# Optimization experiments

Hardware: AMD Instinct MI355X
Metric: run time of the kernel (lower is better)

The kernel has to match this reference:

```python
import jax, jax.numpy as jnp
import numpy as np

PI = jnp.pi

def phasor_encode(x):
    # map phase in [-1,1] to unit complex phasor exp(i*pi*x)
    return jnp.exp(jnp.complex64(1j) * PI * x.astype(jnp.float32))

def phasor_act(z):
    # angle of complex activation, normalized back to [-1,1]
    return jnp.angle(z) / PI

def multi_dense(x, w, b):
    # PhasorMultiDense: x [b,t,d], w [h,d,D], b [h,D] (complex bias, ones init)
    xz = phasor_encode(x)                                      # [b,t,d] complex64
    wz = w.astype(jnp.complex64)
    bz = b.astype(jnp.complex64)
    yz = jnp.einsum('btd,hdD->bhtD', xz, wz) + bz[None, :, None, :]
    return phasor_act(yz)                                      # [b,h,t,D] real

def attend(q, k, v):
    # VSA phasor attention: similarity = Re(qz . conj(kz)) / d, softmax, complex bundle of v phasors
    d = q.shape[-1]
    qz = phasor_encode(q)
    kz = phasor_encode(k)
    scores = jnp.real(jnp.einsum('bhtd,bhTd->bhtT', qz, jnp.conj(kz))) / d
    probs = jax.nn.softmax(scores, axis=-1)
    vz = phasor_encode(v)
    out = jnp.einsum('bhtT,bhTd->bhtd', probs.astype(jnp.complex64), vz)
    return phasor_act(out)                                     # [b,h,t,D]

def setup_inputs() -> dict:
    key = jax.random.key(0)
    ks = jax.random.split(key, 8)
    B, Tq, Tkv, D, H = 2, 1024, 1024, 512, 8
    sw = 1.0 / np.sqrt(D)       # VarianceScaling(1.0) fan_in
    swo = 1.0 / np.sqrt(H * D)
    return {
        'query': jax.random.uniform(ks[0], (B, Tq, D), jnp.float32, -1.0, 1.0),
        'keyvalue': jax.random.uniform(ks[1], (B, Tkv, D), jnp.float32, -1.0, 1.0),
        'wq': jax.random.normal(ks[2], (H, D, D), jnp.float32) * sw,
        'bq': jnp.ones((H, D), jnp.float32),
        'wk': jax.random.normal(ks[3], (H, D, D), jnp.float32) * sw,
        'bk': jnp.ones((H, D), jnp.float32),
        'wv': jax.random.normal(ks[4], (H, D, D), jnp.float32) * sw,
        'bv': jnp.ones((H, D), jnp.float32),
        'wo': jax.random.normal(ks[5], (H * D, D), jnp.float32) * swo,
        'bo': jnp.ones((D,), jnp.float32),
    }

def reference(query, keyvalue, wq, bq, wk, bk, wv, bv, wo, bo):
    q = multi_dense(query, wq, bq)        # [b,h,t,D]
    k = multi_dense(keyvalue, wk, bk)
    v = multi_dense(keyvalue, wv, bv)
    r = attend(q, k, v)                   # [b,h,t,D]
    b_, h_, t_, d_ = r.shape
    r_flat = jnp.transpose(r, (0, 2, 1, 3)).reshape(b_, t_, h_ * d_)  # b t (h d)
    # final PhasorDense
    xz = phasor_encode(r_flat)
    z = jnp.einsum('btd,dD->btD', xz, wo.astype(jnp.complex64)) + bo.astype(jnp.complex64)
    return phasor_act(z)                  # [b, t_q, output_channels]
```

## Files before the change

kernel.cpp:

```cpp
#include <hip/hip_runtime.h>
#include <math.h>


#define PI_F 3.14159274101257324f

typedef __attribute__((ext_vector_type(8))) _Float16 half8;
typedef __attribute__((ext_vector_type(4))) _Float16 half4;
typedef __attribute__((ext_vector_type(2))) _Float16 half2v;
typedef __attribute__((ext_vector_type(16))) float f32x16;
typedef unsigned int u32;

#define MFMA32(a, b, c) __builtin_amdgcn_mfma_f32_32x32x16_f16((a), (b), (c), 0, 0, 0)
#define ROWOF(r, ln) (((r) & 3) + 8 * ((r) >> 2) + 4 * ((ln) >> 5))

__device__ __forceinline__ void gll16(const void* g, void* l) {
    __builtin_amdgcn_global_load_lds(
        (const __attribute__((address_space(1))) u32*)g,
        (__attribute__((address_space(3))) u32*)l, 16, 0, 0);
}

__device__ __forceinline__ void split2(float x, _Float16& h, _Float16& l) {
    _Float16 hh = (_Float16)x;
    h = hh;
    l = (_Float16)((x - (float)hh) * 4096.0f);
}

__device__ __forceinline__ int xcdswz(int bid, int nwg) {
    const int cpx = nwg >> 3;
    return (bid & 7) * cpx + (bid >> 3);
}

__global__ __launch_bounds__(256) void encode_phasor(
    const float* __restrict__ xq, const float* __restrict__ xkv,
    _Float16* __restrict__ qch, _Float16* __restrict__ qcl,
    _Float16* __restrict__ qsh, _Float16* __restrict__ qsl,
    _Float16* __restrict__ kch, _Float16* __restrict__ kcl,
    _Float16* __restrict__ ksh, _Float16* __restrict__ ksl)
{
    const int mt = blockIdx.x, yh = blockIdx.y, zi = blockIdx.z;
    const float* x = zi ? xkv : xq;
    __shared__ char fb[32768];
    const int tid = threadIdx.x;
    const int row = tid >> 3, lc = tid & 7;
    const float* xr = x + (size_t)(mt * 32 + row) * 512 + yh * 256;
    for (int c = 0; c < 2; ++c) {
        if (c) __syncthreads();
        half8 hs[4][2];
#pragma unroll
        for (int g = 0; g < 2; ++g)
#pragma unroll
            for (int q = 0; q < 2; ++q) {
                float4 v = *(const float4*)(xr + c * 128 + lc * 16 + g * 8 + q * 4);
                float cc[4], ss[4];
                sincosf(PI_F * v.x, &ss[0], &cc[0]);
                sincosf(PI_F * v.y, &ss[1], &cc[1]);
                sincosf(PI_F * v.z, &ss[2], &cc[2]);
                sincosf(PI_F * v.w, &ss[3], &cc[3]);
#pragma unroll
                for (int e = 0; e < 4; ++e) {
                    _Float16 a, b;
                    split2(cc[e], a, b); hs[0][g][q * 4 + e] = a; hs[1][g][q * 4 + e] = b;
                    split2(ss[e], a, b); hs[2][g][q * 4 + e] = a; hs[3][g][q * 4 + e] = b;
                }
            }
#pragma unroll
        for (int p = 0; p < 4; ++p) {
            char* base = fb + p * 8192 + lc * 1024 + row * 16;
            *(half8*)(base) = hs[p][0];
            *(half8*)(base + 512) = hs[p][1];
        }
        __syncthreads();
#pragma unroll
        for (int w = 0; w < 8; ++w) {
            const int u = w * 256 + tid;
            const int p = u >> 9, rest = u & 511;
            const int f = rest >> 6, within = rest & 63;
            _Float16* op;
            if (zi) op = (p == 0) ? kch : (p == 1) ? kcl : (p == 2) ? ksh : ksl;
            else    op = (p == 0) ? qch : (p == 1) ? qcl : (p == 2) ? qsh : qsl;
            const size_t fragG = (size_t)mt * 32 + yh * 16 + c * 8 + f;
            *(half8*)(op + fragG * 512 + within * 8) =
                *(const half8*)(fb + p * 8192 + f * 1024 + within * 16);
        }
    }
}

__global__ __launch_bounds__(256) void tsplit64(
    const float* __restrict__ w, _Float16* __restrict__ th, _Float16* __restrict__ tl,
    int K, int N)
{
    const int kt = blockIdx.x, ntile = blockIdx.y, h = blockIdx.z;
    const int k0 = kt * 64, n0 = ntile * 64;
    __shared__ float T[64][65];
    const int tid = threadIdx.x;
    const float* wb = w + (size_t)h * K * N;
    {
        const int r = tid >> 4, c4 = (tid & 15) * 4;
#pragma unroll
        for (int rr = 0; rr < 64; rr += 16) {
            float4 v = *(const float4*)&wb[(size_t)(k0 + rr + r) * N + n0 + c4];
            T[rr + r][c4 + 0] = v.x; T[rr + r][c4 + 1] = v.y;
            T[rr + r][c4 + 2] = v.z; T[rr + r][c4 + 3] = v.w;
        }
    }
    __syncthreads();
    {
        const int n = n0 + (tid >> 2), kq = k0 + (tid & 3) * 16;
        half8 hv[2], lv[2];
#pragma unroll
        for (int q = 0; q < 16; ++q) {
            float f = T[kq - k0 + q][n - n0];
            _Float16 hh, ll; split2(f, hh, ll);
            hv[q >> 3][q & 7] = hh; lv[q >> 3][q & 7] = ll;
        }
        const size_t hb = (size_t)h * 512 * K;
        const size_t offA = hb + ((size_t)((n >> 5) * (K >> 4) + (kq >> 4))) * 512
                            + (n & 31) * 8;
        *(half8*)(th + offA) = hv[0]; *(half8*)(th + offA + 256) = hv[1];
        *(half8*)(tl + offA) = lv[0]; *(half8*)(tl + offA + 256) = lv[1];
    }
}

__global__ __launch_bounds__(256) void tsplit_qkv(
    const float* __restrict__ wq, const float* __restrict__ wk,
    const float* __restrict__ wv,
    _Float16* __restrict__ qh, _Float16* __restrict__ ql,
    _Float16* __restrict__ kh, _Float16* __restrict__ kl,
    _Float16* __restrict__ vh, _Float16* __restrict__ vl, int hcnt)
{
    const int tsel = blockIdx.z / hcnt, h = blockIdx.z % hcnt;
    const int kt = blockIdx.x, ntile = blockIdx.y;
    const int k0 = kt * 64, n0 = ntile * 64;
    const float* w = (tsel == 0) ? wq : (tsel == 1) ? wk : wv;
    _Float16* th = (tsel == 0) ? qh : (tsel == 1) ? kh : vh;
    _Float16* tl = (tsel == 0) ? ql : (tsel == 1) ? kl : vl;
    __shared__ float T[64][65];
    const int tid = threadIdx.x;
    const float* wb = w + (size_t)h * 262144;
    {
        const int r = tid >> 4, c4 = (tid & 15) * 4;
#pragma unroll
        for (int rr = 0; rr < 64; rr += 16) {
            float4 v = *(const float4*)&wb[(size_t)(k0 + rr + r) * 512 + n0 + c4];
            T[rr + r][c4 + 0] = v.x; T[rr + r][c4 + 1] = v.y;
            T[rr + r][c4 + 2] = v.z; T[rr + r][c4 + 3] = v.w;
        }
    }
    __syncthreads();
    {
        const int n = n0 + (tid >> 2), kq = k0 + (tid & 3) * 16;
        half8 hv[2], lv[2];
#pragma unroll
        for (int q = 0; q < 16; ++q) {
            float f = T[kq - k0 + q][n - n0];
            _Float16 hh, ll; split2(f, hh, ll);
            hv[q >> 3][q & 7] = hh; lv[q >> 3][q & 7] = ll;
        }
        const size_t hb = (size_t)h * 262144;
        const size_t offA = hb + ((size_t)((n >> 5) * 32 + (kq >> 4))) * 512 + (n & 31) * 8;
        *(half8*)(th + offA) = hv[0]; *(half8*)(th + offA + 256) = hv[1];
        *(half8*)(tl + offA) = lv[0]; *(half8*)(tl + offA + 256) = lv[1];
    }
}

__global__ __launch_bounds__(256, 2) void proj_qk(
    const _Float16* __restrict__ qch, const _Float16* __restrict__ qcl,
    const _Float16* __restrict__ qsh, const _Float16* __restrict__ qsl,
    const _Float16* __restrict__ kch, const _Float16* __restrict__ kcl,
    const _Float16* __restrict__ ksh, const _Float16* __restrict__ ksl,
    const _Float16* __restrict__ wqh, const _Float16* __restrict__ wql,
    const _Float16* __restrict__ wkh, const _Float16* __restrict__ wkl,
    const float* __restrict__ bq, const float* __restrict__ bk,
    _Float16* __restrict__ qzh, _Float16* __restrict__ qzl,
    _Float16* __restrict__ kzh, _Float16* __restrict__ kzl,
    int h0, int hcnt)
{
    const int inp = blockIdx.z;
    const _Float16* xch = inp ? kch : qch;
    const _Float16* xcl = inp ? kcl : qcl;
    const _Float16* xsh = inp ? ksh : qsh;
    const _Float16* xsl = inp ? ksl : qsl;
    const _Float16* wth = inp ? wkh : wqh;
    const _Float16* wtl = inp ? wkl : wql;
    const float* bias = inp ? bk : bq;
    _Float16* ozh = inp ? kzh : qzh;
    _Float16* ozl = inp ? kzl : qzl;

    const int m0 = blockIdx.x * 64;
    const int hc = blockIdx.y >> 2;
    const int n0 = (blockIdx.y & 3) * 128;
    __shared__ char lds[32768];
    const int tid = threadIdx.x, wv = tid >> 6, ln = tid & 63;
    const int wr = wv >> 1, wc = wv & 1, lm32 = ln & 31;

    const size_t abase = ((size_t)((m0 >> 5) + wr)) * 32 * 512 + ln * 8;
    const _Float16* pxc[2] = { xch + abase, xcl + abase };
    const _Float16* pxs[2] = { xsh + abase, xsl + abase };

    const char* spB[4]; int dpB[4];
#pragma unroll
    for (int u = 0; u < 4; ++u) {
        const int g = wv * 4 + u;
        const int jt = g >> 2, hl = (g >> 1) & 1, ks = g & 1;
        const _Float16* base = (hl ? wtl : wth) + (size_t)hc * 262144;
        spB[u] = (const char*)(base
                 + ((size_t)(((n0 + jt * 32) >> 5) * 32 + ks)) * 512 + ln * 8);
        dpB[u] = g * 1024;
    }

    f32x16 ach[2] = {}, acl[2] = {}, ash[2] = {}, asl[2] = {};

    auto LOADA = [&](int s, half8 (&ac)[2][2], half8 (&as)[2][2]) {
#pragma unroll
        for (int hl = 0; hl < 2; ++hl)
#pragma unroll
            for (int ks = 0; ks < 2; ++ks) {
                ac[hl][ks] = *(const half8*)(pxc[hl] + (2 * s + ks) * 512);
                as[hl][ks] = *(const half8*)(pxs[hl] + (2 * s + ks) * 512);
            }
    };
    auto STAGEB = [&](int s, int buf) {
#pragma unroll
        for (int u = 0; u < 4; ++u)
            gll16(spB[u] + (size_t)s * 2048, lds + buf + dpB[u]);
    };
    auto MSTEP = [&](int buf, half8 (&ac)[2][2], half8 (&as)[2][2]) {
        half8 w0[2][2], w1[2][2];
#pragma unroll
        for (int ks = 0; ks < 2; ++ks)
#pragma unroll
            for (int j = 0; j < 2; ++j) {
                const int gb = (wc * 2 + j) * 4 + ks;
                w0[ks][j] = *(const half8*)(lds + buf + gb * 1024 + ln * 16);
                w1[ks][j] = *(const half8*)(lds + buf + (gb + 2) * 1024 + ln * 16);
            }
        __builtin_amdgcn_s_setprio(1);
#pragma unroll
        for (int ks = 0; ks < 2; ++ks)
#pragma unroll
            for (int j = 0; j < 2; ++j) {
                ach[j] = MFMA32(ac[0][ks], w0[ks][j], ach[j]);
                acl[j] = MFMA32(ac[0][ks], w1[ks][j], acl[j]);
                acl[j] = MFMA32(ac[1][ks], w0[ks][j], acl[j]);
                ash[j] = MFMA32(as[0][ks], w0[ks][j], ash[j]);
                asl[j] = MFMA32(as[0][ks], w1[ks][j], asl[j]);
                asl[j] = MFMA32(as[1][ks], w0[ks][j], asl[j]);
            }
        __builtin_amdgcn_s_setprio(0);
    };

    half8 Ac0[2][2], As0[2][2], Ac1[2][2], As1[2][2];
    LOADA(0, Ac0, As0); STAGEB(0, 0);
    const int NS = 16;
    for (int s = 0; s < NS; s += 2) {
        __syncthreads();
        STAGEB(s + 1, 16384); LOADA(s + 1, Ac1, As1);
        MSTEP(0, Ac0, As0);
        __syncthreads();
        if (s + 2 < NS) { STAGEB(s + 2, 0); LOADA(s + 2, Ac0, As0); }
        MSTEP(16384, Ac1, As1);
    }

    const float LS = 1.0f / 4096.0f;
    const int b = m0 >> 10, tbase = m0 & 1023;
    const size_t zz = (size_t)(b * hcnt + hc);
    const size_t zb = zz << 20;
    __syncthreads();
#pragma unroll
    for (int p = 0; p < 2; ++p) {
        if (p) __syncthreads();
#pragma unroll
        for (int j = 0; j < 2; ++j) {
            const int nloc = wc * 64 + j * 32 + lm32;
            const float bval = bias[(size_t)(h0 + hc) * 512 + n0 + nloc];
            const int kk = 2 * nloc;
#pragma unroll
            for (int r = 0; r < 16; ++r) {
                const int mloc = wr * 32 + ROWOF(r, ln);
                float yc = ach[j][r] + acl[j][r] * LS + bval;
                float ys = ash[j][r] + asl[j][r] * LS;
                float inv = 1.0f / sqrtf(fmaxf(yc * yc + ys * ys, 1e-36f));
                _Float16 c_h, c_l, s_h, s_l;
                split2(yc * inv, c_h, c_l);
                split2(ys * inv, s_h, s_l);
                half2v pr;
                pr[0] = p ? c_l : c_h;
                pr[1] = p ? s_l : s_h;
                *(half2v*)(lds + ((mloc >> 5) * 16 + (kk >> 4)) * 1024
                    + (mloc & 31) * 16 + 512 * ((kk >> 3) & 1) + (kk & 7) * 2) = pr;
            }
        }
        __syncthreads();
        _Float16* op = p ? ozl : ozh;
#pragma unroll
        for (int w = 0; w < 8; ++w) {
            const int u = w * 256 + tid;
            const int f = u >> 6, within = u & 63;
            const int ms = f >> 4, kf = f & 15;
            *(half8*)(op + zb + (((size_t)(tbase >> 5) + ms) * 64 + (n0 >> 3) + kf) * 512
                      + within * 8) = *(const half8*)(lds + f * 1024 + within * 16);
        }
    }
}

__global__ __launch_bounds__(256, 2) void proj_v(
    const _Float16* __restrict__ xch, const _Float16* __restrict__ xcl,
    const _Float16* __restrict__ xsh, const _Float16* __restrict__ xsl,
    const _Float16* __restrict__ wth, const _Float16* __restrict__ wtl,
    const float* __restrict__ bias,
    _Float16* __restrict__ vc_h, _Float16* __restrict__ vc_l,
    _Float16* __restrict__ vs_h, _Float16* __restrict__ vs_l,
    int h0, int hcnt)
{
    const int m0 = blockIdx.x * 64;
    const int hc = blockIdx.y >> 2;
    const int n0 = (blockIdx.y & 3) * 128;
    __shared__ char lds[32768];
    const int tid = threadIdx.x, wv = tid >> 6, ln = tid & 63;
    const int wr = wv >> 1, wc = wv & 1, lm32 = ln & 31;

    const size_t abase = ((size_t)((m0 >> 5) + wr)) * 32 * 512 + ln * 8;
    const _Float16* pxc[2] = { xch + abase, xcl + abase };
    const _Float16* pxs[2] = { xsh + abase, xsl + abase };

    const char* spB[4]; int dpB[4];
#pragma unroll
    for (int u = 0; u < 4; ++u) {
        const int g = wv * 4 + u;
        const int jt = g >> 2, hl = (g >> 1) & 1, ks = g & 1;
        const _Float16* base = (hl ? wtl : wth) + (size_t)hc * 262144;
        spB[u] = (const char*)(base
                 + ((size_t)(((n0 + jt * 32) >> 5) * 32 + ks)) * 512 + ln * 8);
        dpB[u] = g * 1024;
    }

    f32x16 ach[2] = {}, acl[2] = {}, ash[2] = {}, asl[2] = {};

    auto LOADA = [&](int s, half8 (&ac)[2][2], half8 (&as)[2][2]) {
#pragma unroll
        for (int hl = 0; hl < 2; ++hl)
#pragma unroll
            for (int ks = 0; ks < 2; ++ks) {
                ac[hl][ks] = *(const half8*)(pxc[hl] + (2 * s + ks) * 512);
                as[hl][ks] = *(const half8*)(pxs[hl] + (2 * s + ks) * 512);
            }
    };
    auto STAGEB = [&](int s, int buf) {
#pragma unroll
        for (int u = 0; u < 4; ++u)
            gll16(spB[u] + (size_t)s * 2048, lds + buf + dpB[u]);
    };
    auto MSTEP = [&](int buf, half8 (&ac)[2][2], half8 (&as)[2][2]) {
        half8 w0[2][2], w1[2][2];
#pragma unroll
        for (int ks = 0; ks < 2; ++ks)
#pragma unroll
            for (int j = 0; j < 2; ++j) {
                const int gb = (wc * 2 + j) * 4 + ks;
                w0[ks][j] = *(const half8*)(lds + buf + gb * 1024 + ln * 16);
                w1[ks][j] = *(const half8*)(lds + buf + (gb + 2) * 1024 + ln * 16);
            }
        __builtin_amdgcn_s_setprio(1);
#pragma unroll
        for (int ks = 0; ks < 2; ++ks)
#pragma unroll
            for (int j = 0; j < 2; ++j) {
                ach[j] = MFMA32(ac[0][ks], w0[ks][j], ach[j]);
                acl[j] = MFMA32(ac[0][ks], w1[ks][j], acl[j]);
                acl[j] = MFMA32(ac[1][ks], w0[ks][j], acl[j]);
                ash[j] = MFMA32(as[0][ks], w0[ks][j], ash[j]);
                asl[j] = MFMA32(as[0][ks], w1[ks][j], asl[j]);
                asl[j] = MFMA32(as[1][ks], w0[ks][j], asl[j]);
            }
        __builtin_amdgcn_s_setprio(0);
    };

    half8 Ac0[2][2], As0[2][2], Ac1[2][2], As1[2][2];
    LOADA(0, Ac0, As0); STAGEB(0, 0);
    const int NS = 16;
    for (int s = 0; s < NS; s += 2) {
        __syncthreads();
        STAGEB(s + 1, 16384); LOADA(s + 1, Ac1, As1);
        MSTEP(0, Ac0, As0);
        __syncthreads();
        if (s + 2 < NS) { STAGEB(s + 2, 0); LOADA(s + 2, Ac0, As0); }
        MSTEP(16384, Ac1, As1);
    }

    const float LS = 1.0f / 4096.0f;
    const int b = m0 >> 10, tbase = m0 & 1023;
    const size_t zz = (size_t)(b * hcnt + hc);
    const size_t zvb = zz * 524288;
    _Float16* T = (_Float16*)lds;
#pragma unroll
    for (int p = 0; p < 4; ++p) {
        __syncthreads();
#pragma unroll
        for (int j = 0; j < 2; ++j) {
            const int dloc = wc * 64 + j * 32 + lm32;
            const float bval = bias[(size_t)(h0 + hc) * 512 + n0 + dloc];
#pragma unroll
            for (int r = 0; r < 16; ++r) {
                const int tloc = wr * 32 + ROWOF(r, ln);
                float yc = ach[j][r] + acl[j][r] * LS + bval;
                float ys = ash[j][r] + asl[j][r] * LS;
                float inv = 1.0f / sqrtf(fmaxf(yc * yc + ys * ys, 1e-36f));
                _Float16 hh, ll;
                if (p < 2) split2(yc * inv, hh, ll);
                else       split2(ys * inv, hh, ll);
                T[dloc * 80 + tloc] = (p & 1) ? ll : hh;
            }
        }
        __syncthreads();
        _Float16* op = (p == 0) ? vc_h : (p == 1) ? vc_l : (p == 2) ? vs_h : vs_l;
#pragma unroll
        for (int w = 0; w < 4; ++w) {
            const int u = w * 256 + tid;
            const int f = u >> 6, within = u & 63;
            const int ds_ = f >> 2, tf = f & 3;
            const int d = ds_ * 32 + (within & 31);
            const int tl = tf * 16 + (within >> 5) * 8;
            half8 vv = *(const half8*)(T + d * 80 + tl);
            *(half8*)(op + zvb + (((size_t)((n0 >> 5) + ds_)) * 64 + (tbase >> 4) + tf) * 512
                      + within * 8) = vv;
        }
    }
}

__global__ __launch_bounds__(256, 2) void scores_mfma(
    const _Float16* __restrict__ qzh, const _Float16* __restrict__ qzl,
    const _Float16* __restrict__ kzh, const _Float16* __restrict__ kzl,
    float* __restrict__ S, int Z)
{
    const int wg = xcdswz(blockIdx.x, Z * 64);
    const int z = wg >> 6;
    const int rem = wg & 63;
    const int m0 = (rem & 7) << 7, n0 = (rem >> 3) << 7;
    __shared__ char lds[32768];
    const size_t zb = (size_t)z << 20;
    const int tid = threadIdx.x, wv = tid >> 6, ln = tid & 63;
    const int wr = wv >> 1, wc = wv & 1, lm32 = ln & 31;

    const _Float16* pa[2] = { qzh + zb + ln * 8, qzl + zb + ln * 8 };
    const char* spB[4]; int dpB[4];
#pragma unroll
    for (int u = 0; u < 4; ++u) {
        const int g = wv * 4 + u;
        const int jt = g >> 2, hl = (g >> 1) & 1, ks = g & 1;
        spB[u] = (const char*)((hl ? kzl : kzh) + zb
                 + ((size_t)(((n0 + jt * 32) >> 5) * 64 + ks)) * 512 + ln * 8);
        dpB[u] = g * 1024;
    }

    f32x16 acch[2][2] = {}, accl[2][2] = {};

    auto LOADA = [&](int s, half8 (&a)[2][2][2]) {
#pragma unroll
        for (int hl = 0; hl < 2; ++hl)
#pragma unroll
            for (int i = 0; i < 2; ++i)
#pragma unroll
                for (int ks = 0; ks < 2; ++ks)
                    a[hl][i][ks] = *(const half8*)(pa[hl]
                        + ((size_t)((m0 >> 5) + wr * 2 + i) * 64 + 2 * s + ks) * 512);
    };
    auto STAGEB = [&](int s, int buf) {
#pragma unroll
        for (int u = 0; u < 4; ++u)
            gll16(spB[u] + (size_t)s * 2048, lds + buf + dpB[u]);
    };
    auto MSTEP = [&](int buf, half8 (&a)[2][2][2]) {
        half8 bh[2][2], bl[2][2];
#pragma unroll
        for (int ks = 0; ks < 2; ++ks)
#pragma unroll
            for (int j = 0; j < 2; ++j) {
                const int gb = (wc * 2 + j) * 4 + ks;
                bh[ks][j] = *(const half8*)(lds + buf + gb * 1024 + ln * 16);
                bl[ks][j] = *(const half8*)(lds + buf + (gb + 2) * 1024 + ln * 16);
            }
        __builtin_amdgcn_s_setprio(1);
#pragma unroll
        for (int ks = 0; ks < 2; ++ks)
#pragma unroll
            for (int i = 0; i < 2; ++i)
#pragma unroll
                for (int j = 0; j < 2; ++j) {
                    acch[i][j] = MFMA32(a[0][i][ks], bh[ks][j], acch[i][j]);
                    accl[i][j] = MFMA32(a[0][i][ks], bl[ks][j], accl[i][j]);
                    accl[i][j] = MFMA32(a[1][i][ks], bh[ks][j], accl[i][j]);
                }
        __builtin_amdgcn_s_setprio(0);
    };

    half8 A0[2][2][2], A1[2][2][2];
    LOADA(0, A0); STAGEB(0, 0);
    const int NS = 32;
    for (int s = 0; s < NS; s += 2) {
        __syncthreads();
        STAGEB(s + 1, 16384); LOADA(s + 1, A1);
        MSTEP(0, A0);
        __syncthreads();
        if (s + 2 < NS) { STAGEB(s + 2, 0); LOADA(s + 2, A0); }
        MSTEP(16384, A1);
    }
    const float LS = 1.0f / 4096.0f, SC = 1.0f / 512.0f;
#pragma unroll
    for (int i = 0; i < 2; ++i)
#pragma unroll
        for (int j = 0; j < 2; ++j)
#pragma unroll
            for (int r = 0; r < 16; ++r) {
                const int row = m0 + wr * 64 + i * 32 + ROWOF(r, ln);
                const int col = n0 + wc * 64 + j * 32 + lm32;
                S[zb + (size_t)row * 1024 + col] =
                    (acch[i][j][r] + accl[i][j][r] * LS) * SC;
            }
}

__global__ __launch_bounds__(256) void softmax_frag(
    const float* __restrict__ S, _Float16* __restrict__ Ph, _Float16* __restrict__ Pl)
{
    const int z = blockIdx.x >> 5, tt = blockIdx.x & 31;
    const float* Sb = S + ((size_t)z << 20) + ((size_t)tt << 15);
    const int tid = threadIdx.x;
    const int row = tid >> 3, lc = tid & 7;
    __shared__ float rsum[32];
    __shared__ char fb[32768];
    const float* prow = Sb + (size_t)row * 1024 + lc * 128;
    float s = 0.f;
    for (int q = 0; q < 32; ++q) {
        float4 v = *(const float4*)(prow + q * 4);
        s += (expf(v.x) + expf(v.y)) + (expf(v.z) + expf(v.w));
    }
    s += __shfl_xor(s, 1); s += __shfl_xor(s, 2); s += __shfl_xor(s, 4);
    if (lc == 0) rsum[row] = s;
    __syncthreads();
    const float inv = 1.0f / rsum[row];
    for (int c = 0; c < 4; ++c) {
        if (c) __syncthreads();
        const float* pc = Sb + (size_t)row * 1024 + c * 256 + lc * 32;
#pragma unroll
        for (int q = 0; q < 8; ++q) {
            float4 v = *(const float4*)(pc + q * 4);
            half4 hv, lv; _Float16 a, b;
            split2(expf(v.x) * inv, a, b); hv[0] = a; lv[0] = b;
            split2(expf(v.y) * inv, a, b); hv[1] = a; lv[1] = b;
            split2(expf(v.z) * inv, a, b); hv[2] = a; lv[2] = b;
            split2(expf(v.w) * inv, a, b); hv[3] = a; lv[3] = b;
            const int f = lc * 2 + (q >> 2);
            const int boff = f * 1024 + row * 16 + 512 * ((q >> 1) & 1) + (q & 1) * 8;
            *(half4*)(fb + boff) = hv;
            *(half4*)(fb + 16384 + boff) = lv;
        }
        __syncthreads();
#pragma unroll
        for (int w = 0; w < 8; ++w) {
            const int u = w * 256 + tid;
            const int pl = u >> 10, rest = u & 1023;
            const int f = rest >> 6, within = rest & 63;
            _Float16* dst = (pl ? Pl : Ph) + ((size_t)z << 20)
                          + ((size_t)(tt * 64 + c * 16 + f)) * 512 + within * 8;
            *(half8*)dst = *(const half8*)(fb + pl * 16384 + f * 1024 + within * 16);
        }
    }
}

__global__ __launch_bounds__(256, 2) void pv_mfma(
    const _Float16* __restrict__ Ph, const _Float16* __restrict__ Pl,
    const _Float16* __restrict__ vch, const _Float16* __restrict__ vcl,
    const _Float16* __restrict__ vsh, const _Float16* __restrict__ vsl,
    _Float16* __restrict__ rch, _Float16* __restrict__ rcl,
    _Float16* __restrict__ rsh, _Float16* __restrict__ rsl,
    int h0, int hcnt, int Z)
{
    const int wg = xcdswz(blockIdx.x, Z * 64);
    const int z = wg >> 6;
    const int rem = wg & 63;
    const int m0 = (rem & 7) << 7, n0 = (rem >> 3) << 6;
    __shared__ char lds[32768];
    const int tid = threadIdx.x, wv = tid >> 6, ln = tid & 63;
    const int wr = wv >> 1, wc = wv & 1, lm32 = ln & 31;

    const size_t zb = (size_t)z << 20, zvb = (size_t)z * 524288;
    const _Float16* pa[2] = { Ph + zb + ln * 8, Pl + zb + ln * 8 };
    const char* spB[4]; int dpB[4];
#pragma unroll
    for (int u = 0; u < 4; ++u) {
        const int g = wv * 4 + u;
        const int pl = g >> 3, dt = (g >> 2) & 1, hl = (g >> 1) & 1, ks = g & 1;
        const _Float16* base = pl ? (hl ? vsl : vsh) : (hl ? vcl : vch);
        spB[u] = (const char*)(base + zvb
                 + ((size_t)(((n0 + dt * 32) >> 5) * 64 + ks)) * 512 + ln * 8);
        dpB[u] = g * 1024;
    }

    f32x16 ac_h[2] = {}, ac_l[2] = {}, as_h[2] = {}, as_l[2] = {};

    auto LOADA = [&](int s, half8 (&a)[2][2][2]) {
#pragma unroll
        for (int hl = 0; hl < 2; ++hl)
#pragma unroll
            for (int i = 0; i < 2; ++i)
#pragma unroll
                for (int ks = 0; ks < 2; ++ks)
                    a[hl][i][ks] = *(const half8*)(pa[hl]
                        + ((size_t)((m0 >> 5) + wr * 2 + i) * 64 + 2 * s + ks) * 512);
    };
    auto STAGEB = [&](int s, int buf) {
#pragma unroll
        for (int u = 0; u < 4; ++u)
            gll16(spB[u] + (size_t)s * 2048, lds + buf + dpB[u]);
    };
    auto MSTEP = [&](int buf, half8 (&a)[2][2][2]) {
        half8 vc[2][2], vs[2][2];
#pragma unroll
        for (int hl = 0; hl < 2; ++hl)
#pragma unroll
            for (int ks = 0; ks < 2; ++ks) {
                vc[hl][ks] = *(const half8*)(lds + buf + (wc * 4 + hl * 2 + ks) * 1024 + ln * 16);
                vs[hl][ks] = *(const half8*)(lds + buf + (8 + wc * 4 + hl * 2 + ks) * 1024 + ln * 16);
            }
        __builtin_amdgcn_s_setprio(1);
#pragma unroll
        for (int ks = 0; ks < 2; ++ks)
#pragma unroll
            for (int i = 0; i < 2; ++i) {
                ac_h[i] = MFMA32(a[0][i][ks], vc[0][ks], ac_h[i]);
                ac_l[i] = MFMA32(a[0][i][ks], vc[1][ks], ac_l[i]);
                ac_l[i] = MFMA32(a[1][i][ks], vc[0][ks], ac_l[i]);
                as_h[i] = MFMA32(a[0][i][ks], vs[0][ks], as_h[i]);
                as_l[i] = MFMA32(a[0][i][ks], vs[1][ks], as_l[i]);
                as_l[i] = MFMA32(a[1][i][ks], vs[0][ks], as_l[i]);
            }
        __builtin_amdgcn_s_setprio(0);
    };

    half8 A0[2][2][2], A1[2][2][2];
    LOADA(0, A0); STAGEB(0, 0);
    const int NS = 32;
    for (int s = 0; s < NS; s += 2) {
        __syncthreads();
        STAGEB(s + 1, 16384); LOADA(s + 1, A1);
        MSTEP(0, A0);
        __syncthreads();
        if (s + 2 < NS) { STAGEB(s + 2, 0); LOADA(s + 2, A0); }
        MSTEP(16384, A1);
    }
    const float LS = 1.0f / 4096.0f;
    const int b = z / hcnt, hg = h0 + z % hcnt;
    const size_t mrow = (size_t)((b * 1024 + m0) >> 5);
    const size_t kcol = (size_t)(hg * 512 + n0) >> 4;
    __syncthreads();
#pragma unroll
    for (int p = 0; p < 4; ++p) {
        if (p) __syncthreads();
#pragma unroll
        for (int i = 0; i < 2; ++i)
#pragma unroll
            for (int r = 0; r < 16; ++r) {
                const int mloc = wr * 64 + i * 32 + ROWOF(r, ln);
                const int kloc = wc * 32 + lm32;
                float zc = ac_h[i][r] + ac_l[i][r] * LS;
                float zs = as_h[i][r] + as_l[i][r] * LS;
                float inv = 1.0f / sqrtf(fmaxf(zc * zc + zs * zs, 1e-36f));
                _Float16 hh, ll;
                if (p < 2) split2(zc * inv, hh, ll);
                else       split2(zs * inv, hh, ll);
                *(_Float16*)(lds + ((mloc >> 5) * 4 + (kloc >> 4)) * 1024
                    + (mloc & 31) * 16 + 512 * ((kloc >> 3) & 1) + (kloc & 7) * 2)
                    = (p & 1) ? ll : hh;
            }
        __syncthreads();
        _Float16* op = (p == 0) ? rch : (p == 1) ? rcl : (p == 2) ? rsh : rsl;
#pragma unroll
        for (int w = 0; w < 4; ++w) {
            const int u = w * 256 + tid;
            const int f = u >> 6, within = u & 63;
            const int ms = f >> 2, kf = f & 3;
            *(half8*)(op + ((mrow + ms) * 256 + kcol + kf) * 512 + within * 8)
                = *(const half8*)(lds + f * 1024 + within * 16);
        }
    }
}

__global__ __launch_bounds__(256, 2) void final_mfma(
    const _Float16* __restrict__ rch, const _Float16* __restrict__ rcl,
    const _Float16* __restrict__ rsh, const _Float16* __restrict__ rsl,
    const _Float16* __restrict__ woh, const _Float16* __restrict__ wol,
    float* __restrict__ pbuf)
{
    const int m0 = blockIdx.x * 64, n0 = blockIdx.y * 128;
    const int kspl = blockIdx.z;
    const int kf = kspl * 64;
    __shared__ char lds[32768];
    const int tid = threadIdx.x, wv = tid >> 6, ln = tid & 63;
    const int wr = wv >> 1, wc = wv & 1, lm32 = ln & 31;

    const size_t abase = ((size_t)((m0 >> 5) + wr) * 256 + kf) * 512 + ln * 8;
    const _Float16* prc[2] = { rch + abase, rcl + abase };
    const _Float16* prs[2] = { rsh + abase, rsl + abase };
    const char* spB[4]; int dpB[4];
#pragma unroll
    for (int u = 0; u < 4; ++u) {
        const int g = wv * 4 + u;
        const int jt = g >> 2, hl = (g >> 1) & 1, ks = g & 1;
        spB[u] = (const char*)((hl ? wol : woh)
                 + ((size_t)(((n0 + jt * 32) >> 5) * 256 + kf + ks)) * 512 + ln * 8);
        dpB[u] = g * 1024;
    }

    f32x16 rr_h[2] = {}, rr_l[2] = {}, ri_h[2] = {}, ri_l[2] = {};

    auto LOADA = [&](int s, half8 (&ac)[2][2], half8 (&as)[2][2]) {
#pragma unroll
        for (int hl = 0; hl < 2; ++hl)
#pragma unroll
            for (int ks = 0; ks < 2; ++ks) {
                ac[hl][ks] = *(const half8*)(prc[hl] + (2 * s + ks) * 512);
                as[hl][ks] = *(const half8*)(prs[hl] + (2 * s + ks) * 512);
            }
    };
    auto STAGEB = [&](int s, int buf) {
#pragma unroll
        for (int u = 0; u < 4; ++u)
            gll16(spB[u] + (size_t)s * 2048, lds + buf + dpB[u]);
    };
    auto MSTEP = [&](int buf, half8 (&ac)[2][2], half8 (&as)[2][2]) {
        half8 w0[2][2], w1[2][2];
#pragma unroll
        for (int ks = 0; ks < 2; ++ks)
#pragma unroll
            for (int j = 0; j < 2; ++j) {
                const int gb = (wc * 2 + j) * 4 + ks;
                w0[ks][j] = *(const half8*)(lds + buf + gb * 1024 + ln * 16);
                w1[ks][j] = *(const half8*)(lds + buf + (gb + 2) * 1024 + ln * 16);
            }
        __builtin_amdgcn_s_setprio(1);
#pragma unroll
        for (int ks = 0; ks < 2; ++ks)
#pragma unroll
            for (int j = 0; j < 2; ++j) {
                rr_h[j] = MFMA32(ac[0][ks], w0[ks][j], rr_h[j]);
                rr_l[j] = MFMA32(ac[0][ks], w1[ks][j], rr_l[j]);
                rr_l[j] = MFMA32(ac[1][ks], w0[ks][j], rr_l[j]);
                ri_h[j] = MFMA32(as[0][ks], w0[ks][j], ri_h[j]);
                ri_l[j] = MFMA32(as[0][ks], w1[ks][j], ri_l[j]);
                ri_l[j] = MFMA32(as[1][ks], w0[ks][j], ri_l[j]);
            }
        __builtin_amdgcn_s_setprio(0);
    };

    half8 Ac0[2][2], As0[2][2], Ac1[2][2], As1[2][2];
    LOADA(0, Ac0, As0); STAGEB(0, 0);
    const int NS = 32;
    for (int s = 0; s < NS; s += 2) {
        __syncthreads();
        STAGEB(s + 1, 16384); LOADA(s + 1, Ac1, As1);
        MSTEP(0, Ac0, As0);
        __syncthreads();
        if (s + 2 < NS) { STAGEB(s + 2, 0); LOADA(s + 2, Ac0, As0); }
        MSTEP(16384, Ac1, As1);
    }
    const float LS = 1.0f / 4096.0f;
#pragma unroll
    for (int j = 0; j < 2; ++j) {
        const int ng = n0 + wc * 64 + j * 32 + lm32;
#pragma unroll
        for (int r = 0; r < 16; ++r) {
            const int mg = m0 + wr * 32 + ROWOF(r, ln);
            float2 v;
            v.x = rr_h[j][r] + rr_l[j][r] * LS;
            v.y = ri_h[j][r] + ri_l[j][r] * LS;
            *(float2*)&pbuf[((size_t)(kspl * 2048 + mg) * 512 + ng) * 2] = v;
        }
    }
}

__global__ __launch_bounds__(256) void final_combine(
    const float* __restrict__ pbuf, const float* __restrict__ bo,
    float* __restrict__ out, int KS)
{
    const int m = blockIdx.x, t = threadIdx.x;
    float4 acc = {0.f, 0.f, 0.f, 0.f};
    for (int s = 0; s < KS; ++s) {
        float4 v = *(const float4*)&pbuf[(size_t)(s * 2048 + m) * 1024 + t * 4];
        acc.x += v.x; acc.y += v.y; acc.z += v.z; acc.w += v.w;
    }
    const int n0 = t * 2;
    out[(size_t)m * 512 + n0]     = atan2f(acc.y, acc.x + bo[n0]) / PI_F;
    out[(size_t)m * 512 + n0 + 1] = atan2f(acc.w, acc.z + bo[n0 + 1]) / PI_F;
}

extern "C" void kernel_launch(void* const* d_in, const int* in_sizes, int n_in,
                              void* d_out, int out_size, void* d_ws, size_t ws_size,
                              hipStream_t stream)
{
    (void)in_sizes; (void)n_in; (void)out_size;
    const float* query    = (const float*)d_in[0];
    const float* keyvalue = (const float*)d_in[1];
    const float* wq = (const float*)d_in[2];
    const float* bq = (const float*)d_in[3];
    const float* wk = (const float*)d_in[4];
    const float* bk = (const float*)d_in[5];
    const float* wv = (const float*)d_in[6];
    const float* bv = (const float*)d_in[7];
    const float* wo = (const float*)d_in[8];
    const float* bo = (const float*)d_in[9];
    float* out = (float*)d_out;

    int hcnt;
    if (ws_size >= (size_t)320 * 1024 * 1024) hcnt = 8;
    else if (ws_size >= (size_t)240 * 1024 * 1024) hcnt = 4;
    else hcnt = 2;
    const int Z = 2 * hcnt;
    const int KS = (hcnt == 2) ? 2 : 4;

    char* p = (char*)d_ws;
    auto alloc = [&](size_t bytes) {
        char* r = p;
        p += (bytes + 255) & ~(size_t)255;
        return r;
    };
    const size_t PLX = (size_t)2048 * 512;
    _Float16* xq[4]; for (int i = 0; i < 4; ++i) xq[i] = (_Float16*)alloc(PLX * 2);
    _Float16* xk[4]; for (int i = 0; i < 4; ++i) xk[i] = (_Float16*)alloc(PLX * 2);
    _Float16* woT[2]; for (int i = 0; i < 2; ++i) woT[i] = (_Float16*)alloc((size_t)512 * 4096 * 2);
    const size_t WTE = (size_t)hcnt * 512 * 512;
    _Float16* wqT[2]; for (int i = 0; i < 2; ++i) wqT[i] = (_Float16*)alloc(WTE * 2);
    _Float16* wkT[2]; for (int i = 0; i < 2; ++i) wkT[i] = (_Float16*)alloc(WTE * 2);
    _Float16* wvT[2]; for (int i = 0; i < 2; ++i) wvT[i] = (_Float16*)alloc(WTE * 2);
    const size_t QZE = (size_t)Z * 1024 * 1024;
    _Float16* qz[2]; for (int i = 0; i < 2; ++i) qz[i] = (_Float16*)alloc(QZE * 2);
    _Float16* kz[2]; for (int i = 0; i < 2; ++i) kz[i] = (_Float16*)alloc(QZE * 2);
    float* S = (float*)alloc(QZE * 4);
    const size_t VTE = (size_t)Z * 512 * 1024;
    _Float16* vT[4]; for (int i = 0; i < 4; ++i) vT[i] = (_Float16*)alloc(VTE * 2);
    const size_t RCE = (size_t)2048 * 4096;
    _Float16* rcs[4];
    if (hcnt == 8) {
        for (int i = 0; i < 4; ++i) rcs[i] = (_Float16*)((char*)qz[0] + (size_t)i * RCE * 2);
    } else {
        for (int i = 0; i < 4; ++i) rcs[i] = (_Float16*)alloc(RCE * 2);
    }
    _Float16* Ph = kz[0];
    _Float16* Pl = kz[1];
    float* pbuf = (float*)kz[0];

    dim3 blk(256);

    encode_phasor<<<dim3(64, 2, 2), blk, 0, stream>>>(
        query, keyvalue,
        xq[0], xq[1], xq[2], xq[3], xk[0], xk[1], xk[2], xk[3]);
    tsplit64<<<dim3(64, 8, 1), blk, 0, stream>>>(wo, woT[0], woT[1], 4096, 512);

    for (int c = 0; c < 8 / hcnt; ++c) {
        const int h0 = c * hcnt;
        tsplit_qkv<<<dim3(8, 8, 3 * hcnt), blk, 0, stream>>>(
            wq + (size_t)h0 * 262144, wk + (size_t)h0 * 262144, wv + (size_t)h0 * 262144,
            wqT[0], wqT[1], wkT[0], wkT[1], wvT[0], wvT[1], hcnt);

        proj_qk<<<dim3(32, hcnt * 4, 2), blk, 0, stream>>>(
            xq[0], xq[1], xq[2], xq[3], xk[0], xk[1], xk[2], xk[3],
            wqT[0], wqT[1], wkT[0], wkT[1], bq, bk,
            qz[0], qz[1], kz[0], kz[1], h0, hcnt);
        proj_v<<<dim3(32, hcnt * 4), blk, 0, stream>>>(
            xk[0], xk[1], xk[2], xk[3], wvT[0], wvT[1], bv,
            vT[0], vT[1], vT[2], vT[3], h0, hcnt);

        scores_mfma<<<dim3(Z * 64), blk, 0, stream>>>(qz[0], qz[1], kz[0], kz[1], S, Z);
        softmax_frag<<<dim3(Z * 32), blk, 0, stream>>>(S, Ph, Pl);
        pv_mfma<<<dim3(Z * 64), blk, 0, stream>>>(
            Ph, Pl, vT[0], vT[1], vT[2], vT[3],
            rcs[0], rcs[1], rcs[2], rcs[3], h0, hcnt, Z);
    }

    final_mfma<<<dim3(32, 4, KS), blk, 0, stream>>>(
        rcs[0], rcs[1], rcs[2], rcs[3], woT[0], woT[1], pbuf);
    final_combine<<<dim3(2048), blk, 0, stream>>>(pbuf, bo, out, KS);
}
```

Before: 587.1 us.

## Fuse exponentiation into scores kernel and drop softmax normalization pass

The scores kernel now exponentiates its accumulators, splits them into high and low fp16 halves, and writes the probability fragments directly in the layout pv_mfma expects. This removes the fp32 score matrix round-trip through global memory and the separate softmax kernel launch. The row-sum division is dropped because the final angle() is invariant to positive scaling of each row. Max-subtraction is also skipped, which relies on the scores being bounded in [-1,1]. The P buffers get their own allocation instead of aliasing kz.

```diff
diff --git a/kernel.cpp b/kernel.cpp
--- a/kernel.cpp
+++ b/kernel.cpp
@@ -430,7 +430,7 @@
 __global__ __launch_bounds__(256, 2) void scores_mfma(
     const _Float16* __restrict__ qzh, const _Float16* __restrict__ qzl,
     const _Float16* __restrict__ kzh, const _Float16* __restrict__ kzl,
-    float* __restrict__ S, int Z)
+    _Float16* __restrict__ Ph, _Float16* __restrict__ Pl, int Z)
 {
     const int wg = xcdswz(blockIdx.x, Z * 64);
     const int z = wg >> 6;
@@ -504,64 +504,37 @@
         if (s + 2 < NS) { STAGEB(s + 2, 0); LOADA(s + 2, A0); }
         MSTEP(16384, A1);
     }
+
     const float LS = 1.0f / 4096.0f, SC = 1.0f / 512.0f;
-#pragma unroll
-    for (int i = 0; i < 2; ++i)
-#pragma unroll
-        for (int j = 0; j < 2; ++j)
-#pragma unroll
-            for (int r = 0; r < 16; ++r) {
-                const int row = m0 + wr * 64 + i * 32 + ROWOF(r, ln);
-                const int col = n0 + wc * 64 + j * 32 + lm32;
-                S[zb + (size_t)row * 1024 + col] =
-                    (acch[i][j][r] + accl[i][j][r] * LS) * SC;
-            }
-}
-
-__global__ __launch_bounds__(256) void softmax_frag(
-    const float* __restrict__ S, _Float16* __restrict__ Ph, _Float16* __restrict__ Pl)
-{
-    const int z = blockIdx.x >> 5, tt = blockIdx.x & 31;
-    const float* Sb = S + ((size_t)z << 20) + ((size_t)tt << 15);
-    const int tid = threadIdx.x;
-    const int row = tid >> 3, lc = tid & 7;
-    __shared__ float rsum[32];
-    __shared__ char fb[32768];
-    const float* prow = Sb + (size_t)row * 1024 + lc * 128;
-    float s = 0.f;
-    for (int q = 0; q < 32; ++q) {
-        float4 v = *(const float4*)(prow + q * 4);
-        s += (expf(v.x) + expf(v.y)) + (expf(v.z) + expf(v.w));
-    }
-    s += __shfl_xor(s, 1); s += __shfl_xor(s, 2); s += __shfl_xor(s, 4);
-    if (lc == 0) rsum[row] = s;
     __syncthreads();
-    const float inv = 1.0f / rsum[row];
-    for (int c = 0; c < 4; ++c) {
-        if (c) __syncthreads();
-        const float* pc = Sb + (size_t)row * 1024 + c * 256 + lc * 32;
-#pragma unroll
-        for (int q = 0; q < 8; ++q) {
-            float4 v = *(const float4*)(pc + q * 4);
-            half4 hv, lv; _Float16 a, b;
-            split2(expf(v.x) * inv, a, b); hv[0] = a; lv[0] = b;
-            split2(expf(v.y) * inv, a, b); hv[1] = a; lv[1] = b;
-            split2(expf(v.z) * inv, a, b); hv[2] = a; lv[2] = b;
-            split2(expf(v.w) * inv, a, b); hv[3] = a; lv[3] = b;
-            const int f = lc * 2 + (q >> 2);
-            const int boff = f * 1024 + row * 16 + 512 * ((q >> 1) & 1) + (q & 1) * 8;
-            *(half4*)(fb + boff) = hv;
-            *(half4*)(fb + 16384 + boff) = lv;
-        }
-        __syncthreads();
+#pragma unroll
+    for (int p = 0; p < 2; ++p) {
+        if (p) __syncthreads();
+#pragma unroll
+        for (int i = 0; i < 2; ++i)
+#pragma unroll
+            for (int j = 0; j < 2; ++j)
+#pragma unroll
+                for (int r = 0; r < 16; ++r) {
+                    const int tl = wr * 64 + i * 32 + ROWOF(r, ln);
+                    const int Tl = wc * 64 + j * 32 + lm32;
+                    float Pv = expf((acch[i][j][r] + accl[i][j][r] * LS) * SC);
+                    _Float16 hh, ll;
+                    split2(Pv, hh, ll);
+                    const int fl = (tl >> 5) * 8 + (Tl >> 4);
+                    *(_Float16*)(lds + fl * 1024 + (tl & 31) * 16
+                        + 512 * ((Tl >> 3) & 1) + (Tl & 7) * 2) = p ? ll : hh;
+                }
+        __syncthreads();
+        _Float16* op = p ? Pl : Ph;
 #pragma unroll
         for (int w = 0; w < 8; ++w) {
             const int u = w * 256 + tid;
-            const int pl = u >> 10, rest = u & 1023;
-            const int f = rest >> 6, within = rest & 63;
-            _Float16* dst = (pl ? Pl : Ph) + ((size_t)z << 20)
-                          + ((size_t)(tt * 64 + c * 16 + f)) * 512 + within * 8;
-            *(half8*)dst = *(const half8*)(fb + pl * 16384 + f * 1024 + within * 16);
+            const int f = u >> 6, l = u & 63;
+            const int ft = f >> 3, fT = f & 7;
+            const size_t dst = zb + ((size_t)(((m0 >> 5) + ft) * 64
+                               + (n0 >> 4) + fT)) * 512 + l * 8;
+            *(half8*)(op + dst) = *(const half8*)(lds + f * 1024 + l * 16);
         }
     }
 }
@@ -833,7 +806,8 @@
     const size_t QZE = (size_t)Z * 1024 * 1024;
     _Float16* qz[2]; for (int i = 0; i < 2; ++i) qz[i] = (_Float16*)alloc(QZE * 2);
     _Float16* kz[2]; for (int i = 0; i < 2; ++i) kz[i] = (_Float16*)alloc(QZE * 2);
-    float* S = (float*)alloc(QZE * 4);
+    _Float16* Ph = (_Float16*)alloc(QZE * 2);
+    _Float16* Pl = (_Float16*)alloc(QZE * 2);
     const size_t VTE = (size_t)Z * 512 * 1024;
     _Float16* vT[4]; for (int i = 0; i < 4; ++i) vT[i] = (_Float16*)alloc(VTE * 2);
     const size_t RCE = (size_t)2048 * 4096;
@@ -843,9 +817,7 @@
     } else {
         for (int i = 0; i < 4; ++i) rcs[i] = (_Float16*)alloc(RCE * 2);
     }
-    _Float16* Ph = kz[0];
-    _Float16* Pl = kz[1];
-    float* pbuf = (float*)kz[0];
+    float* pbuf = (float*)Ph;
 
     dim3 blk(256);
 
@@ -868,8 +840,8 @@
             xk[0], xk[1], xk[2], xk[3], wvT[0], wvT[1], bv,
             vT[0], vT[1], vT[2], vT[3], h0, hcnt);
 
-        scores_mfma<<<dim3(Z * 64), blk, 0, stream>>>(qz[0], qz[1], kz[0], kz[1], S, Z);
-        softmax_frag<<<dim3(Z * 32), blk, 0, stream>>>(S, Ph, Pl);
+        scores_mfma<<<dim3(Z * 64), blk, 0, stream>>>(
+            qz[0], qz[1], kz[0], kz[1], Ph, Pl, Z);
         pv_mfma<<<dim3(Z * 64), blk, 0, stream>>>(
             Ph, Pl, vT[0], vT[1], vT[2], vT[3],
             rcs[0], rcs[1], rcs[2], rcs[3], h0, hcnt, Z);
```

New measurement: 548.7 us, median of 2. 6.5% less time.
